# Optimization experiments

Hardware: AMD Instinct MI355X
Metric: run time of the kernel (lower is better)

Reference implementation:

```python
import jax, jax.numpy as jnp
import numpy as np

EMBED_DIM = 1024
NUM_HEADS = 16
HEAD_DIM = EMBED_DIM // NUM_HEADS


def setup_inputs() -> dict:
    key = jax.random.key(0)
    ks = jax.random.split(key, 7)
    B, S, D = 2, 2048, EMBED_DIM
    s = 1.0 / np.sqrt(D)
    return {
        "x": jax.random.normal(ks[0], (B, S, D), dtype=jnp.float32),
        "Wq": jax.random.normal(ks[1], (D, D), dtype=jnp.float32) * s,
        "bq": jax.random.normal(ks[2], (D,), dtype=jnp.float32) * 0.01,
        "Wk": jax.random.normal(ks[3], (D, D), dtype=jnp.float32) * s,
        "bk": jax.random.normal(ks[4], (D,), dtype=jnp.float32) * 0.01,
        "Wv": jax.random.normal(ks[5], (D, D), dtype=jnp.float32) * s,
        "bv": jax.random.normal(ks[6], (D,), dtype=jnp.float32) * 0.01,
    }


def reference(x, Wq, bq, Wk, bk, Wv, bv):
    B, S, D = x.shape
    H, Hd = NUM_HEADS, HEAD_DIM
    # QKV projections, then split heads: [B, S, D] -> [B, H, S, Hd]
    q = (x @ Wq + bq).reshape(B, S, H, Hd).transpose(0, 2, 1, 3)
    k = (x @ Wk + bk).reshape(B, S, H, Hd).transpose(0, 2, 1, 3)
    v = (x @ Wv + bv).reshape(B, S, H, Hd).transpose(0, 2, 1, 3)
    # NOTE: the original module applies NO 1/sqrt(head_dim) scaling.
    energy = jnp.einsum("bhqd,bhkd->bhqk", q, k)  # [B, H, S, S]
    attn = jax.nn.softmax(energy, axis=-1)
    out = jnp.einsum("bhqk,bhkd->bhqd", attn, v)
    return out.transpose(0, 2, 1, 3).reshape(B, S, D)
```

## Files before the change

### kernel.cpp

```cpp
#include <hip/hip_runtime.h>
#include <stdint.h>
#include <stddef.h>

typedef _Float16 half_t;
typedef __attribute__((ext_vector_type(8))) _Float16 h16x8;
typedef __attribute__((ext_vector_type(4))) _Float16 h16x4;
typedef __attribute__((ext_vector_type(4))) float f32x4;

#define MFMA16(a, b, c) __builtin_amdgcn_mfma_f32_16x16x32_f16(a, b, c, 0, 0, 0)
#define EXP2(x) __builtin_amdgcn_exp2f(x)

#define SW(row, slot) ((((slot) ^ ((row) & 7))) * 8)

__global__ __launch_bounds__(256) void cvt_x_kernel(const float* __restrict__ x,
                                                    half_t* __restrict__ xh, int n8) {
    int i = blockIdx.x * blockDim.x + threadIdx.x;
    if (i >= n8) return;
    const float4* xv = (const float4*)x;
    float4 a = xv[i * 2 + 0];
    float4 b = xv[i * 2 + 1];
    h16x8 o;
    o[0] = (half_t)a.x; o[1] = (half_t)a.y; o[2] = (half_t)a.z; o[3] = (half_t)a.w;
    o[4] = (half_t)b.x; o[5] = (half_t)b.y; o[6] = (half_t)b.z; o[7] = (half_t)b.w;
    ((h16x8*)xh)[i] = o;
}

__global__ __launch_bounds__(256) void cvt_w_kernel(const float* __restrict__ Wq,
                                                    const float* __restrict__ Wk,
                                                    const float* __restrict__ Wv,
                                                    half_t* __restrict__ Wt) {
    __shared__ float t[32][33];
    const float* W = (blockIdx.z == 0) ? Wq : ((blockIdx.z == 1) ? Wk : Wv);
    int k0 = blockIdx.y * 32, n0 = blockIdx.x * 32;
    int tid = threadIdx.x;
    int r = tid >> 3;
    int c4 = (tid & 7) * 4;
    float4 v = *(const float4*)&W[(size_t)(k0 + r) * 1024 + n0 + c4];
    t[r][c4 + 0] = v.x; t[r][c4 + 1] = v.y; t[r][c4 + 2] = v.z; t[r][c4 + 3] = v.w;
    __syncthreads();
    half_t* o = Wt + (size_t)blockIdx.z * 1024 * 1024 + (size_t)(n0 + r) * 1024 + k0 + c4;
    h16x4 h;
    h[0] = (half_t)t[c4 + 0][r];
    h[1] = (half_t)t[c4 + 1][r];
    h[2] = (half_t)t[c4 + 2][r];
    h[3] = (half_t)t[c4 + 3][r];
    *(h16x4*)o = h;
}

__global__ __launch_bounds__(256, 2) void gemm_qkv_kernel(
    const half_t* __restrict__ xh,
    const half_t* __restrict__ Wt,
    const float* __restrict__ bq, const float* __restrict__ bk,
    const float* __restrict__ bv,
    half_t* __restrict__ qkv)
{
    const int p = blockIdx.z;
    const float* bias = (p == 0) ? bq : ((p == 1) ? bk : bv);
    const half_t* Wp = Wt + (size_t)p * 1024 * 1024;
    const int n0 = blockIdx.x * 128, m0 = blockIdx.y * 128;

    __shared__ half_t Al[128][72];
    __shared__ half_t Bl[128][72];

    const int tid = threadIdx.x;
    const int lane = tid & 63, wid = tid >> 6;
    const int wm = wid >> 1, wn = wid & 1;
    const int g = lane >> 4, r = lane & 15;

    const int srow = tid >> 3;
    const int scol = (tid & 7) * 8;

    f32x4 acc[4][4];
#pragma unroll
    for (int a = 0; a < 4; a++)
#pragma unroll
        for (int c = 0; c < 4; c++) acc[a][c] = (f32x4){0.f, 0.f, 0.f, 0.f};

    h16x8 ra[4], rb[4];
#pragma unroll
    for (int i = 0; i < 4; i++) {
        ra[i] = *(const h16x8*)&xh[(size_t)(m0 + srow + i * 32) * 1024 + scol];
        rb[i] = *(const h16x8*)&Wp[(size_t)(n0 + srow + i * 32) * 1024 + scol];
    }

    for (int k0 = 0; k0 < 1024; k0 += 64) {
        __syncthreads();
#pragma unroll
        for (int i = 0; i < 4; i++) {
            *(h16x8*)&Al[srow + i * 32][scol] = ra[i];
            *(h16x8*)&Bl[srow + i * 32][scol] = rb[i];
        }
        __syncthreads();

        int kn = (k0 + 64) & 1023;
#pragma unroll
        for (int i = 0; i < 4; i++) {
            ra[i] = *(const h16x8*)&xh[(size_t)(m0 + srow + i * 32) * 1024 + kn + scol];
            rb[i] = *(const h16x8*)&Wp[(size_t)(n0 + srow + i * 32) * 1024 + kn + scol];
        }

#pragma unroll
        for (int t = 0; t < 2; t++) {
            h16x8 af[4], bf[4];
#pragma unroll
            for (int mi = 0; mi < 4; mi++)
                af[mi] = *(const h16x8*)&Al[wm * 64 + mi * 16 + r][t * 32 + g * 8];
#pragma unroll
            for (int ni = 0; ni < 4; ni++)
                bf[ni] = *(const h16x8*)&Bl[wn * 64 + ni * 16 + r][t * 32 + g * 8];
#pragma unroll
            for (int mi = 0; mi < 4; mi++)
#pragma unroll
                for (int ni = 0; ni < 4; ni++)
                    acc[mi][ni] = MFMA16(af[mi], bf[ni], acc[mi][ni]);
        }
    }

    float bn[4];
#pragma unroll
    for (int ni = 0; ni < 4; ni++) bn[ni] = bias[n0 + wn * 64 + ni * 16 + r];

    if (p == 0) {
        half_t* outp = qkv;
#pragma unroll
        for (int mi = 0; mi < 4; mi++) {
#pragma unroll
            for (int ni = 0; ni < 4; ni++) {
                int n = n0 + wn * 64 + ni * 16 + r;
                int hq = n >> 6, hd = n & 63;
#pragma unroll
                for (int i = 0; i < 4; i++) {
                    int m = m0 + wm * 64 + mi * 16 + g * 4 + i;
                    int b = m >> 11, s = m & 2047;
                    outp[(((size_t)(b * 16 + hq) * 2048 + s) << 6) + hd] =
                        (half_t)(acc[mi][ni][i] + bn[ni]);
                }
            }
        }
    } else if (p == 1) {
        half_t* outp = qkv + (size_t)4194304;
        const int kt = ((m0 & 2047) + wm * 64) >> 6;
        const int bK = (m0 + wm * 64) >> 11;
#pragma unroll
        for (int ni = 0; ni < 4; ni++) {
            int n = n0 + wn * 64 + ni * 16 + r;
            int hK = n >> 6, hd = n & 63;
            int tt = hd >> 5, ggk = (hd >> 3) & 3, jK = hd & 7;
            size_t base = (size_t)(bK * 16 + hK) * 131072 + kt * 4096 + tt * 512 + ggk * 128 + jK;
#pragma unroll
            for (int mi = 0; mi < 4; mi++)
#pragma unroll
                for (int i = 0; i < 4; i++)
                    outp[base + mi * 1024 + (g * 4 + i) * 8] =
                        (half_t)(acc[mi][ni][i] + bn[ni]);
        }
    } else {
        half_t* outp = qkv + (size_t)2 * 4194304;
        const int kt = ((m0 & 2047) + wm * 64) >> 6;
        const int bV = (m0 + wm * 64) >> 11;
        const int jv = (g & 1) * 4, gv_hi = g >> 1;
#pragma unroll
        for (int ni = 0; ni < 4; ni++) {
            int n = n0 + wn * 64 + ni * 16 + r;
            int hV = n >> 6;
            size_t hb = (size_t)(bV * 16 + hV) * 131072 + kt * 4096 + ni * 1024;
#pragma unroll
            for (int mi = 0; mi < 4; mi++) {
                int ks = mi >> 1, ggv = (mi & 1) * 2 + gv_hi;
                h16x4 pk;
#pragma unroll
                for (int i = 0; i < 4; i++) pk[i] = (half_t)(acc[mi][ni][i] + bn[ni]);
                *(h16x4*)&outp[hb + ks * 512 + ggv * 128 + r * 8 + jv] = pk;
            }
        }
    }
}

__global__ __launch_bounds__(256, 2) void attn_kernel(
    const half_t* __restrict__ Qg,
    const half_t* __restrict__ Kswz,
    const half_t* __restrict__ Vswz,
    float* __restrict__ out)
{
    __shared__ half_t Pl[4][32][64];

    const int tid = threadIdx.x;
    const int lane = tid & 63, wid = tid >> 6;
    const int g = lane >> 4, r = lane & 15;

    const int bid = blockIdx.x;
    const int xcd = bid & 7;
    const int t_  = bid >> 3;
    const int qblk = t_ & 15;
    const int bh = xcd + 8 * (t_ >> 4);

    const int b = bh >> 4, h = bh & 15;
    const half_t* Qb = Qg + (size_t)bh * 131072;
    const half_t* Kp = Kswz + (size_t)bh * 131072;
    const half_t* Vp = Vswz + (size_t)bh * 131072;
    const int q0 = qblk * 128 + wid * 32;
    const int lofs = g * 128 + r * 8;

    h16x8 qf[2][2];
#pragma unroll
    for (int qg = 0; qg < 2; qg++)
#pragma unroll
        for (int t = 0; t < 2; t++) {
            qf[qg][t] = *(const h16x8*)&Qb[(size_t)(q0 + qg * 16 + r) * 64 + t * 32 + g * 8];
            qf[qg][t] *= (half_t)1.44269504f;
        }

    f32x4 o[2][4];
#pragma unroll
    for (int qg = 0; qg < 2; qg++)
#pragma unroll
        for (int d = 0; d < 4; d++) o[qg][d] = (f32x4){0.f, 0.f, 0.f, 0.f};
    float m_run[2] = {0.f, 0.f}, l_run[2] = {0.f, 0.f};

    auto loadK = [&](int kt, h16x8* kf) {
#pragma unroll
        for (int kc = 0; kc < 4; kc++)
#pragma unroll
            for (int t = 0; t < 2; t++)
                kf[kc * 2 + t] = *(const h16x8*)&Kp[kt * 4096 + kc * 1024 + t * 512 + lofs];
    };
    auto loadV = [&](int kt, h16x8* vf) {
#pragma unroll
        for (int d = 0; d < 4; d++)
#pragma unroll
            for (int ks = 0; ks < 2; ks++)
                vf[d * 2 + ks] = *(const h16x8*)&Vp[kt * 4096 + d * 1024 + ks * 512 + lofs];
    };

    h16x8 kf[8], vf[8];
    loadK(0, kf);

    for (int kt = 0; kt < 32; ++kt) {
        loadV(kt, vf);

        f32x4 e[2][4];
#pragma unroll
        for (int kc = 0; kc < 4; kc++) {
            e[0][kc] = (f32x4){0.f, 0.f, 0.f, 0.f};
            e[1][kc] = (f32x4){0.f, 0.f, 0.f, 0.f};
#pragma unroll
            for (int t = 0; t < 2; t++) {
                e[0][kc] = MFMA16(kf[kc * 2 + t], qf[0][t], e[0][kc]);
                e[1][kc] = MFMA16(kf[kc * 2 + t], qf[1][t], e[1][kc]);
            }
        }

        loadK((kt + 1) & 31, kf);

#pragma unroll
        for (int qg = 0; qg < 2; qg++) {
            float t0 = fmaxf(fmaxf(e[qg][0][0], e[qg][0][1]), e[qg][0][2]);
            float t1 = fmaxf(fmaxf(e[qg][0][3], e[qg][1][0]), e[qg][1][1]);
            float t2 = fmaxf(fmaxf(e[qg][1][2], e[qg][1][3]), e[qg][2][0]);
            float t3 = fmaxf(fmaxf(e[qg][2][1], e[qg][2][2]), e[qg][2][3]);
            float t4 = fmaxf(fmaxf(e[qg][3][0], e[qg][3][1]), e[qg][3][2]);
            float tm = fmaxf(fmaxf(t0, t1), fmaxf(fmaxf(t2, t3), fmaxf(t4, e[qg][3][3])));
            tm = fmaxf(tm, __shfl_xor(tm, 16));
            tm = fmaxf(tm, __shfl_xor(tm, 32));

            float ps0 = 0.f, ps1 = 0.f, ps2 = 0.f, ps3 = 0.f;
#pragma unroll
            for (int i = 0; i < 4; i++) { e[qg][0][i] = EXP2(e[qg][0][i] - m_run[qg]); ps0 += e[qg][0][i]; }
#pragma unroll
            for (int i = 0; i < 4; i++) { e[qg][1][i] = EXP2(e[qg][1][i] - m_run[qg]); ps1 += e[qg][1][i]; }
#pragma unroll
            for (int i = 0; i < 4; i++) { e[qg][2][i] = EXP2(e[qg][2][i] - m_run[qg]); ps2 += e[qg][2][i]; }
#pragma unroll
            for (int i = 0; i < 4; i++) { e[qg][3][i] = EXP2(e[qg][3][i] - m_run[qg]); ps3 += e[qg][3][i]; }

            if (!__all(tm <= m_run[qg] + 8.f)) {
                float nm = fmaxf(m_run[qg], tm);
                float sc = EXP2(m_run[qg] - nm);
                m_run[qg] = nm;
                l_run[qg] *= sc;
#pragma unroll
                for (int kc = 0; kc < 4; kc++)
#pragma unroll
                    for (int i = 0; i < 4; i++) e[qg][kc][i] *= sc;
                ps0 *= sc; ps1 *= sc; ps2 *= sc; ps3 *= sc;
#pragma unroll
                for (int i = 0; i < 4; i++) {
                    float sci = __shfl(sc, (lane & 48) | (g * 4 + i));
#pragma unroll
                    for (int d = 0; d < 4; d++) o[qg][d][i] *= sci;
                }
            }

            float ps = (ps0 + ps1) + (ps2 + ps3);
            ps += __shfl_xor(ps, 16);
            ps += __shfl_xor(ps, 32);
            l_run[qg] += ps;

#pragma unroll
            for (int kc = 0; kc < 4; kc++) {
                h16x4 pk;
#pragma unroll
                for (int i = 0; i < 4; i++) pk[i] = (half_t)e[qg][kc][i];
                *(h16x4*)&Pl[wid][qg * 16 + r][SW(r, 2 * kc + (g >> 1)) + (g & 1) * 4] = pk;
            }
        }
        asm volatile("s_waitcnt lgkmcnt(0)" ::: "memory");
        __builtin_amdgcn_sched_barrier(0);

#pragma unroll
        for (int ks = 0; ks < 2; ks++) {
            h16x8 pf0 = *(const h16x8*)&Pl[wid][r][SW(r, ks * 4 + g)];
            h16x8 pf1 = *(const h16x8*)&Pl[wid][16 + r][SW(r, ks * 4 + g)];
#pragma unroll
            for (int d = 0; d < 4; d++) {
                o[0][d] = MFMA16(pf0, vf[d * 2 + ks], o[0][d]);
                o[1][d] = MFMA16(pf1, vf[d * 2 + ks], o[1][d]);
            }
        }
    }

#pragma unroll
    for (int qg = 0; qg < 2; qg++)
#pragma unroll
        for (int i = 0; i < 4; i++) {
            float li = __shfl(l_run[qg], (lane & 48) | (g * 4 + i));
            float inv = 1.0f / li;
            int s = q0 + qg * 16 + g * 4 + i;
            float* op = out + (size_t)(b * 2048 + s) * 1024 + h * 64 + r;
#pragma unroll
            for (int d = 0; d < 4; d++) op[d * 16] = o[qg][d][i] * inv;
        }
}

extern "C" void kernel_launch(void* const* d_in, const int* in_sizes, int n_in,
                              void* d_out, int out_size, void* d_ws, size_t ws_size,
                              hipStream_t stream) {
    const float* x  = (const float*)d_in[0];
    const float* Wq = (const float*)d_in[1];
    const float* bq = (const float*)d_in[2];
    const float* Wk = (const float*)d_in[3];
    const float* bk = (const float*)d_in[4];
    const float* Wv = (const float*)d_in[5];
    const float* bv = (const float*)d_in[6];
    float* out = (float*)d_out;

    half_t* xh  = (half_t*)d_ws;
    half_t* Wt  = (half_t*)((char*)d_ws + (size_t)8 * 1024 * 1024);
    half_t* qkv = (half_t*)((char*)d_ws + (size_t)14 * 1024 * 1024);
    half_t* Qh  = qkv;
    half_t* Kh  = qkv + (size_t)4194304;
    half_t* Vth = qkv + (size_t)8388608;

    cvt_x_kernel<<<2048, 256, 0, stream>>>(x, xh, 524288);
    cvt_w_kernel<<<dim3(32, 32, 3), 256, 0, stream>>>(Wq, Wk, Wv, Wt);
    gemm_qkv_kernel<<<dim3(8, 32, 3), 256, 0, stream>>>(xh, Wt, bq, bk, bv, qkv);
    attn_kernel<<<512, 256, 0, stream>>>(Qh, Kh, Vth, out);
}
```

Before: 104.9 us.

## Software-pipeline QK^T of the next key tile with softmax of the current one

Splits the attention inner loop into QK^T, softmax/P-write and PV stages, and double-buffers the energy tiles (eA/eB). The QK^T MFMAs for tile kt+1 are then issued before the softmax of tile kt, so matrix-core work can overlap the exp and shuffle work. The per-iteration cross-lane reduction of the row sum is also dropped: each lane keeps a partial sum, reduced once in the epilogue. In exchange, a second set of 32 energy floats stays live, which raises VGPR pressure and may lower occupancy or cause spills.

```diff
diff --git a/kernel.cpp b/kernel.cpp
--- a/kernel.cpp
+++ b/kernel.cpp
@@ -217,14 +217,16 @@
         for (int d = 0; d < 4; d++) o[qg][d] = (f32x4){0.f, 0.f, 0.f, 0.f};
     float m_run[2] = {0.f, 0.f}, l_run[2] = {0.f, 0.f};
 
-    auto loadK = [&](int kt, h16x8* kf) {
+    h16x8 kf[8], vf[8];
+
+    auto loadK = [&](int kt) {
 #pragma unroll
         for (int kc = 0; kc < 4; kc++)
 #pragma unroll
             for (int t = 0; t < 2; t++)
                 kf[kc * 2 + t] = *(const h16x8*)&Kp[kt * 4096 + kc * 1024 + t * 512 + lofs];
     };
-    auto loadV = [&](int kt, h16x8* vf) {
+    auto loadV = [&](int kt) {
 #pragma unroll
         for (int d = 0; d < 4; d++)
 #pragma unroll
@@ -232,13 +234,7 @@
                 vf[d * 2 + ks] = *(const h16x8*)&Vp[kt * 4096 + d * 1024 + ks * 512 + lofs];
     };
 
-    h16x8 kf[8], vf[8];
-    loadK(0, kf);
-
-    for (int kt = 0; kt < 32; ++kt) {
-        loadV(kt, vf);
-
-        f32x4 e[2][4];
+    auto QKT = [&](f32x4 (&e)[2][4]) {
 #pragma unroll
         for (int kc = 0; kc < 4; kc++) {
             e[0][kc] = (f32x4){0.f, 0.f, 0.f, 0.f};
@@ -249,9 +245,9 @@
                 e[1][kc] = MFMA16(kf[kc * 2 + t], qf[1][t], e[1][kc]);
             }
         }
-
-        loadK((kt + 1) & 31, kf);
-
+    };
+
+    auto SOFTMAX_P = [&](f32x4 (&e)[2][4]) {
 #pragma unroll
         for (int qg = 0; qg < 2; qg++) {
             float t0 = fmaxf(fmaxf(e[qg][0][0], e[qg][0][1]), e[qg][0][2]);
@@ -291,10 +287,7 @@
                 }
             }
 
-            float ps = (ps0 + ps1) + (ps2 + ps3);
-            ps += __shfl_xor(ps, 16);
-            ps += __shfl_xor(ps, 32);
-            l_run[qg] += ps;
+            l_run[qg] += (ps0 + ps1) + (ps2 + ps3);
 
 #pragma unroll
             for (int kc = 0; kc < 4; kc++) {
@@ -304,9 +297,11 @@
                 *(h16x4*)&Pl[wid][qg * 16 + r][SW(r, 2 * kc + (g >> 1)) + (g & 1) * 4] = pk;
             }
         }
+    };
+
+    auto PV = [&]() {
         asm volatile("s_waitcnt lgkmcnt(0)" ::: "memory");
         __builtin_amdgcn_sched_barrier(0);
-
 #pragma unroll
         for (int ks = 0; ks < 2; ks++) {
             h16x8 pf0 = *(const h16x8*)&Pl[wid][r][SW(r, ks * 4 + g)];
@@ -317,19 +312,41 @@
                 o[1][d] = MFMA16(pf1, vf[d * 2 + ks], o[1][d]);
             }
         }
-    }
-
-#pragma unroll
-    for (int qg = 0; qg < 2; qg++)
+    };
+
+    f32x4 eA[2][4], eB[2][4];
+    loadK(0);
+    QKT(eA);
+    loadK(1);
+
+    for (int kt = 0; kt < 32; kt += 2) {
+        loadV(kt);
+        QKT(eB);
+        loadK((kt + 2) & 31);
+        SOFTMAX_P(eA);
+        PV();
+        loadV(kt + 1);
+        QKT(eA);
+        loadK((kt + 3) & 31);
+        SOFTMAX_P(eB);
+        PV();
+    }
+
+#pragma unroll
+    for (int qg = 0; qg < 2; qg++) {
+        float lr = l_run[qg];
+        lr += __shfl_xor(lr, 16);
+        lr += __shfl_xor(lr, 32);
 #pragma unroll
         for (int i = 0; i < 4; i++) {
-            float li = __shfl(l_run[qg], (lane & 48) | (g * 4 + i));
+            float li = __shfl(lr, (lane & 48) | (g * 4 + i));
             float inv = 1.0f / li;
             int s = q0 + qg * 16 + g * 4 + i;
             float* op = out + (size_t)(b * 2048 + s) * 1024 + h * 64 + r;
 #pragma unroll
             for (int d = 0; d < 4; d++) op[d * 16] = o[qg][d][i] * inv;
         }
+    }
 }
 
 extern "C" void kernel_launch(void* const* d_in, const int* in_sizes, int n_in,
```

After: 105.2 us. Within noise of the previous version (+0.3%).
